# Kernel tuning notes

Hardware: AMD Instinct MI355X
Metric: run time of the kernel (lower is better)

Reference implementation:

```python
import jax, jax.numpy as jnp
import numpy as np

COMMITMENT_COST = 0.25
N, D, K = 131072, 64, 1024


def setup_inputs() -> dict:
    key = jax.random.key(0)
    k1, k2 = jax.random.split(key)
    inputs = jax.random.normal(k1, (N, D), dtype=jnp.float32)
    # torch init: uniform(-1/K, 1/K)
    weight = jax.random.uniform(k2, (K, D), dtype=jnp.float32,
                                minval=-1.0 / K, maxval=1.0 / K)
    return {"inputs": inputs, "weight": weight}


def reference(inputs, weight):
    x2 = jnp.sum(inputs * inputs, axis=1, keepdims=True)          # [N, 1]
    e2 = jnp.sum(weight * weight, axis=1)                          # [K]
    distances = x2 + e2 - 2.0 * jnp.matmul(inputs, weight.T)       # [N, K]
    encoding_indices = jnp.argmin(distances, axis=1)               # [N]
    # scatter one-hot + matmul in the original == direct gather
    quantized = jnp.take(weight, encoding_indices, axis=0)         # [N, D]
    e_latent_loss = jnp.mean((jax.lax.stop_gradient(quantized) - inputs) ** 2)
    q_latent_loss = jnp.mean((quantized - jax.lax.stop_gradient(inputs)) ** 2)
    loss = q_latent_loss + COMMITMENT_COST * e_latent_loss
    # straight-through estimator
    quantized_st = inputs + jax.lax.stop_gradient(quantized - inputs)
    return (quantized_st, loss, encoding_indices)
```

## Files before the change

### kernel.cpp

```cpp
#include <hip/hip_runtime.h>


#define NROWS 131072
#define DIM 64
#define KCODES 1024
#define MARGIN 5e-5f
#define LOSS_SCALE (1.25f / ((float)NROWS * (float)DIM))

typedef short bf16x8 __attribute__((ext_vector_type(8)));
typedef float f32x4 __attribute__((ext_vector_type(4)));

__device__ __forceinline__ short f2bf(float f) {
    unsigned u = __float_as_uint(f);
    u += 0x7FFF + ((u >> 16) & 1);
    return (short)(u >> 16);
}
__device__ __forceinline__ float bf2f(short h) {
    return __uint_as_float(((unsigned)(unsigned short)h) << 16);
}

__global__ __launch_bounds__(256) void prep_w(const float* __restrict__ w,
                                              float* __restrict__ e2,
                                              short* __restrict__ w_hi,
                                              short* __restrict__ w_lo) {
    int k = blockIdx.x * blockDim.x + threadIdx.x;
    if (k >= KCODES) return;
    const float* wk = w + (size_t)k * DIM;
    float r[DIM];
#pragma unroll
    for (int i = 0; i < DIM / 4; ++i) *(float4*)&r[4 * i] = *(const float4*)(wk + 4 * i);
    float s = 0.f;
#pragma unroll
    for (int d = 0; d < DIM; ++d) s = fmaf(r[d], r[d], s);
    e2[k] = s;

    const int t = k >> 5, ct = (k >> 4) & 1, m = k & 15;
#pragma unroll
    for (int kc = 0; kc < 2; ++kc)
#pragma unroll
        for (int q = 0; q < 4; ++q) {
            bf16x8 hv, lv;
#pragma unroll
            for (int j = 0; j < 8; ++j) {
                float f = r[kc * 32 + q * 8 + j];
                short h = f2bf(f);
                hv[j] = h;
                lv[j] = f2bf(f - bf2f(h));
            }
            size_t fo = ((size_t)(((t * 2 + ct) * 2 + kc) * 4 + q) * 16 + m) * 8;
            *(bf16x8*)(w_hi + fo) = hv;
            *(bf16x8*)(w_lo + fo) = lv;
        }
}

__global__ __launch_bounds__(256, 3) void vq_main(
        const float* __restrict__ x, const float* __restrict__ w,
        const float* __restrict__ e2,
        const short* __restrict__ w_hi, const short* __restrict__ w_lo,
        float* __restrict__ out_q, float* __restrict__ out_loss,
        float* __restrict__ out_idx,
        unsigned* __restrict__ flag_cnt, unsigned* __restrict__ flag_list) {
    const int tid = threadIdx.x;
    const int lane = tid & 63;
    const int wv = tid >> 6;
    const int m = lane & 15;
    const int q = lane >> 4;
    const int block_row0 = blockIdx.x * 128;
    const int wave_row0 = block_row0 + wv * 32;

    __shared__ int sidx[128];
    __shared__ unsigned char sflg[128];
    __shared__ float red[4];

    float xa[2][2][8];
#pragma unroll
    for (int rt = 0; rt < 2; ++rt) {
        const float* xr = x + (size_t)(wave_row0 + rt * 16 + m) * DIM + q * 8;
        *(float4*)&xa[rt][0][0] = *(const float4*)(xr);
        *(float4*)&xa[rt][0][4] = *(const float4*)(xr + 4);
        *(float4*)&xa[rt][1][0] = *(const float4*)(xr + 32);
        *(float4*)&xa[rt][1][4] = *(const float4*)(xr + 36);
    }
    bf16x8 ah[2][2], al[2][2];
#pragma unroll
    for (int rt = 0; rt < 2; ++rt)
#pragma unroll
        for (int c = 0; c < 2; ++c)
#pragma unroll
            for (int j = 0; j < 8; ++j) {
                float f = xa[rt][c][j];
                short h = f2bf(f);
                ah[rt][c][j] = h;
                al[rt][c][j] = f2bf(f - bf2f(h));
            }

    float best[2][4], sec[2][4];
    int bidx[2][4];
#pragma unroll
    for (int rt = 0; rt < 2; ++rt)
#pragma unroll
        for (int r = 0; r < 4; ++r) {
            best[rt][r] = 3.4e38f;
            sec[rt][r] = 3.4e38f;
            bidx[rt][r] = 0;
        }

    const short* ph = w_hi + q * 128 + m * 8;
    const short* pl = w_lo + q * 128 + m * 8;

    for (int t = 0; t < KCODES / 32; ++t) {
        bf16x8 bh[2][2], bl[2][2];
#pragma unroll
        for (int ct = 0; ct < 2; ++ct)
#pragma unroll
            for (int kc = 0; kc < 2; ++kc) {
                int off = t * 2048 + (ct * 2 + kc) * 512;
                bh[ct][kc] = *(const bf16x8*)(ph + off);
                bl[ct][kc] = *(const bf16x8*)(pl + off);
            }
        float e2c0 = e2[t * 32 + m];
        float e2c1 = e2[t * 32 + 16 + m];

        f32x4 acc[2][2];
#pragma unroll
        for (int rt = 0; rt < 2; ++rt)
#pragma unroll
            for (int ct = 0; ct < 2; ++ct) {
                f32x4 a = {0.f, 0.f, 0.f, 0.f};
                a = __builtin_amdgcn_mfma_f32_16x16x32_bf16(al[rt][0], bh[ct][0], a, 0, 0, 0);
                a = __builtin_amdgcn_mfma_f32_16x16x32_bf16(ah[rt][0], bl[ct][0], a, 0, 0, 0);
                a = __builtin_amdgcn_mfma_f32_16x16x32_bf16(ah[rt][0], bh[ct][0], a, 0, 0, 0);
                a = __builtin_amdgcn_mfma_f32_16x16x32_bf16(al[rt][1], bh[ct][1], a, 0, 0, 0);
                a = __builtin_amdgcn_mfma_f32_16x16x32_bf16(ah[rt][1], bl[ct][1], a, 0, 0, 0);
                a = __builtin_amdgcn_mfma_f32_16x16x32_bf16(ah[rt][1], bh[ct][1], a, 0, 0, 0);
                acc[rt][ct] = a;
            }

#pragma unroll
        for (int rt = 0; rt < 2; ++rt)
#pragma unroll
            for (int ct = 0; ct < 2; ++ct) {
                float e2c = ct ? e2c1 : e2c0;
                int id = t * 32 + ct * 16 + m;
#pragma unroll
                for (int r = 0; r < 4; ++r) {
                    float g = fmaf(-2.f, acc[rt][ct][r], e2c);
                    bool c = g < best[rt][r];
                    sec[rt][r] = fminf(sec[rt][r], fmaxf(g, best[rt][r]));
                    if (c) { best[rt][r] = g; bidx[rt][r] = id; }
                }
            }
    }

#pragma unroll
    for (int off = 1; off < 16; off <<= 1)
#pragma unroll
        for (int rt = 0; rt < 2; ++rt)
#pragma unroll
            for (int r = 0; r < 4; ++r) {
                float ob = __shfl_xor(best[rt][r], off, 64);
                int oi = __shfl_xor(bidx[rt][r], off, 64);
                float os = __shfl_xor(sec[rt][r], off, 64);
                float mx = fmaxf(best[rt][r], ob);
                sec[rt][r] = fminf(fminf(sec[rt][r], os), mx);
                bool take = (ob < best[rt][r]) ||
                            (ob == best[rt][r] && oi < bidx[rt][r]);
                if (take) { best[rt][r] = ob; bidx[rt][r] = oi; }
            }

    if (m == 0) {
#pragma unroll
        for (int rt = 0; rt < 2; ++rt)
#pragma unroll
            for (int r = 0; r < 4; ++r) {
                int lr = wv * 32 + rt * 16 + q * 4 + r;
                sidx[lr] = bidx[rt][r];
                bool fl = (sec[rt][r] - best[rt][r]) < MARGIN;
                sflg[lr] = fl ? 1 : 0;
                if (fl) {
                    unsigned p = atomicAdd(flag_cnt, 1u);
                    flag_list[p] = (unsigned)(block_row0 + lr);
                }
            }
    }
    __syncthreads();

    float lsum = 0.f;
    const int rl = tid >> 2, part = tid & 3;
#pragma unroll
    for (int p = 0; p < 2; ++p) {
        int lr = p * 64 + rl;
        int grow = block_row0 + lr;
        if (!sflg[lr]) {
            int bi = sidx[lr];
            const float* xs = x + (size_t)grow * DIM + part * 16;
            const float* ws = w + (size_t)bi * DIM + part * 16;
            float* os = out_q + (size_t)grow * DIM + part * 16;
#pragma unroll
            for (int i = 0; i < 4; ++i) {
                float4 xv = *(const float4*)(xs + 4 * i);
                float4 wv4 = *(const float4*)(ws + 4 * i);
                float d0 = wv4.x - xv.x, d1 = wv4.y - xv.y;
                float d2 = wv4.z - xv.z, d3 = wv4.w - xv.w;
                lsum = fmaf(d0, d0, lsum);
                lsum = fmaf(d1, d1, lsum);
                lsum = fmaf(d2, d2, lsum);
                lsum = fmaf(d3, d3, lsum);
                float4 o = {xv.x + d0, xv.y + d1, xv.z + d2, xv.w + d3};
                *(float4*)(os + 4 * i) = o;
            }
            if (part == 0) out_idx[grow] = (float)bi;
        }
    }

    for (int off = 32; off > 0; off >>= 1) lsum += __shfl_down(lsum, off, 64);
    if ((tid & 63) == 0) red[tid >> 6] = lsum;
    __syncthreads();
    if (tid == 0) {
        float s = (red[0] + red[1]) + (red[2] + red[3]);
        atomicAdd(out_loss, s * LOSS_SCALE);
    }
}

#define CH 16
__global__ __launch_bounds__(256) void vq_cleanup(
        const float* __restrict__ x, const float* __restrict__ w,
        const float* __restrict__ e2,
        const unsigned* __restrict__ flag_cnt,
        const unsigned* __restrict__ flag_list,
        float* __restrict__ out_q, float* __restrict__ out_loss,
        float* __restrict__ out_idx) {
    __shared__ float xs[CH][68];
    __shared__ float wt[128][68];
    __shared__ float sx2[CH];
    const int tid = threadIdx.x;
    const int rowsub = tid >> 4;
    const int kslot = tid & 15;
    const unsigned cnt = *flag_cnt;

    for (unsigned base = blockIdx.x * CH; base < cnt; base += gridDim.x * CH) {
        const int nrows = (int)min((unsigned)CH, cnt - base);
        __syncthreads();
        {
            int rr = tid >> 4, sg = tid & 15;
            if (rr < nrows) {
                unsigned grow = flag_list[base + rr];
                *(float4*)&xs[rr][sg * 4] =
                    *(const float4*)(x + (size_t)grow * DIM + sg * 4);
            }
        }
        __syncthreads();
        if (tid < nrows) {
            float s = 0.f;
#pragma unroll
            for (int d = 0; d < DIM; ++d) s = fmaf(xs[tid][d], xs[tid][d], s);
            sx2[tid] = s;
        }

        unsigned long long kmin = ~0ULL;
        for (int tile = 0; tile < KCODES / 128; ++tile) {
            __syncthreads();
#pragma unroll
            for (int i = 0; i < 8; ++i) {
                int f = tid + i * 256;
                int code = f >> 4, sg = f & 15;
                *(float4*)&wt[code][sg * 4] =
                    *(const float4*)(w + (size_t)(tile * 128 + code) * DIM + sg * 4);
            }
            __syncthreads();
            if (rowsub < nrows) {
#pragma unroll
                for (int j = 0; j < 8; ++j) {
                    int cl = j * 16 + kslot;
                    int code = tile * 128 + cl;
                    float dot = 0.f;
#pragma unroll
                    for (int d4 = 0; d4 < 16; ++d4) {
                        float4 wv4 = *(const float4*)&wt[cl][d4 * 4];
                        float4 xv4 = *(const float4*)&xs[rowsub][d4 * 4];
                        dot = fmaf(wv4.x, xv4.x, dot);
                        dot = fmaf(wv4.y, xv4.y, dot);
                        dot = fmaf(wv4.z, xv4.z, dot);
                        dot = fmaf(wv4.w, xv4.w, dot);
                    }
                    float dist = (sx2[rowsub] + e2[code]) - 2.0f * dot;
                    unsigned long long key =
                        ((unsigned long long)__float_as_uint(dist) << 32) |
                        (unsigned)code;
                    kmin = kmin < key ? kmin : key;
                }
            }
        }
#pragma unroll
        for (int off = 1; off < 16; off <<= 1) {
            unsigned long long o = __shfl_xor(kmin, off, 64);
            kmin = kmin < o ? kmin : o;
        }
        if (rowsub < nrows) {
            int bi = (int)(unsigned)(kmin & 0xFFFFFFFFu);
            unsigned grow = flag_list[base + rowsub];
            float4 x4 = *(float4*)&xs[rowsub][kslot * 4];
            float4 w4 = *(const float4*)(w + (size_t)bi * DIM + kslot * 4);
            float d0 = w4.x - x4.x, d1 = w4.y - x4.y;
            float d2 = w4.z - x4.z, d3 = w4.w - x4.w;
            float ls = 0.f;
            ls = fmaf(d0, d0, ls);
            ls = fmaf(d1, d1, ls);
            ls = fmaf(d2, d2, ls);
            ls = fmaf(d3, d3, ls);
            float4 o = {x4.x + d0, x4.y + d1, x4.z + d2, x4.w + d3};
            *(float4*)(out_q + (size_t)grow * DIM + kslot * 4) = o;
            if (kslot == 0) out_idx[grow] = (float)bi;
#pragma unroll
            for (int off = 1; off < 16; off <<= 1)
                ls += __shfl_xor(ls, off, 64);
            if (kslot == 0) atomicAdd(out_loss, ls * LOSS_SCALE);
        }
    }
}

extern "C" void kernel_launch(void* const* d_in, const int* in_sizes, int n_in,
                              void* d_out, int out_size, void* d_ws, size_t ws_size,
                              hipStream_t stream) {
    const float* x = (const float*)d_in[0];
    const float* w = (const float*)d_in[1];

    float* out_q    = (float*)d_out;
    float* out_loss = (float*)d_out + (size_t)NROWS * DIM;
    float* out_idx  = out_loss + 1;

    float* e2 = (float*)d_ws;
    short* w_hi = (short*)(e2 + KCODES);
    short* w_lo = w_hi + (size_t)KCODES * DIM;
    unsigned* cnt = (unsigned*)(w_lo + (size_t)KCODES * DIM);
    unsigned* list = cnt + 1;

    hipMemsetAsync(out_loss, 0, sizeof(float), stream);
    hipMemsetAsync(cnt, 0, sizeof(unsigned), stream);

    prep_w<<<(KCODES + 255) / 256, 256, 0, stream>>>(w, e2, w_hi, w_lo);
    vq_main<<<NROWS / 128, 256, 0, stream>>>(x, w, e2, w_hi, w_lo,
                                             out_q, out_loss, out_idx, cnt, list);
    vq_cleanup<<<256, 256, 0, stream>>>(x, w, e2, cnt, list,
                                        out_q, out_loss, out_idx);
}
```

Baseline: 208.7 us.

## Pack distance and index into sortable uint key, prefetch codebook tiles, split prep

The argmin tracking now packs the distance's float bits (offset by +0.5 so values are positive and monotone as unsigned) with the 10-bit code index into one unsigned key. This replaces float compare, select and separate index tracking with unsigned min/max, and it also shrinks the shuffle reduction. Codebook fragments and e2 for the next tile are software-prefetched into registers while MFMAs run on the current tile. Weight prep is split into a wide swizzle kernel and a separate e2 kernel. The margin is widened to cover the lost mantissa bits, which sends more rows to the cleanup path, and launch bounds drop to 2 blocks per SM to make room for the extra registers.

```diff
diff --git a/kernel.cpp b/kernel.cpp
--- a/kernel.cpp
+++ b/kernel.cpp
@@ -4,10 +4,11 @@
 #define NROWS 131072
 #define DIM 64
 #define KCODES 1024
-#define MARGIN 5e-5f
+#define MARGIN 2.5e-4f
 #define LOSS_SCALE (1.25f / ((float)NROWS * (float)DIM))
 
 typedef short bf16x8 __attribute__((ext_vector_type(8)));
+typedef short s16x4 __attribute__((ext_vector_type(4)));
 typedef float f32x4 __attribute__((ext_vector_type(4)));
 
 __device__ __forceinline__ short f2bf(float f) {
@@ -19,43 +20,44 @@
     return __uint_as_float(((unsigned)(unsigned short)h) << 16);
 }
 
-__global__ __launch_bounds__(256) void prep_w(const float* __restrict__ w,
-                                              float* __restrict__ e2,
-                                              short* __restrict__ w_hi,
-                                              short* __restrict__ w_lo) {
+__global__ __launch_bounds__(256) void prep_swizzle(const float* __restrict__ w,
+                                                    short* __restrict__ w_hi,
+                                                    short* __restrict__ w_lo) {
+    const int gid = blockIdx.x * 256 + threadIdx.x;
+    const int k = gid >> 4, s = gid & 15;
+    const float4 v = *(const float4*)(w + (size_t)k * DIM + s * 4);
+    const int t = k >> 5, ct = (k >> 4) & 1, m = k & 15;
+    const int kc = s >> 3, q = (s >> 1) & 3, j0 = (s & 1) * 4;
+    const size_t fo =
+        ((size_t)(((t * 2 + ct) * 2 + kc) * 4 + q) * 16 + m) * 8 + j0;
+    float f[4] = {v.x, v.y, v.z, v.w};
+    s16x4 hv, lv;
+#pragma unroll
+    for (int i = 0; i < 4; ++i) {
+        short h = f2bf(f[i]);
+        hv[i] = h;
+        lv[i] = f2bf(f[i] - bf2f(h));
+    }
+    *(s16x4*)(w_hi + fo) = hv;
+    *(s16x4*)(w_lo + fo) = lv;
+}
+
+__global__ __launch_bounds__(256) void prep_e2(const float* __restrict__ w,
+                                               float* __restrict__ e2,
+                                               float* __restrict__ e2p) {
     int k = blockIdx.x * blockDim.x + threadIdx.x;
     if (k >= KCODES) return;
     const float* wk = w + (size_t)k * DIM;
-    float r[DIM];
-#pragma unroll
-    for (int i = 0; i < DIM / 4; ++i) *(float4*)&r[4 * i] = *(const float4*)(wk + 4 * i);
     float s = 0.f;
 #pragma unroll
-    for (int d = 0; d < DIM; ++d) s = fmaf(r[d], r[d], s);
+    for (int d = 0; d < DIM; ++d) s = fmaf(wk[d], wk[d], s);
     e2[k] = s;
-
-    const int t = k >> 5, ct = (k >> 4) & 1, m = k & 15;
-#pragma unroll
-    for (int kc = 0; kc < 2; ++kc)
-#pragma unroll
-        for (int q = 0; q < 4; ++q) {
-            bf16x8 hv, lv;
-#pragma unroll
-            for (int j = 0; j < 8; ++j) {
-                float f = r[kc * 32 + q * 8 + j];
-                short h = f2bf(f);
-                hv[j] = h;
-                lv[j] = f2bf(f - bf2f(h));
-            }
-            size_t fo = ((size_t)(((t * 2 + ct) * 2 + kc) * 4 + q) * 16 + m) * 8;
-            *(bf16x8*)(w_hi + fo) = hv;
-            *(bf16x8*)(w_lo + fo) = lv;
-        }
-}
-
-__global__ __launch_bounds__(256, 3) void vq_main(
+    e2p[k] = s + 0.5f;
+}
+
+__global__ __launch_bounds__(256, 2) void vq_main(
         const float* __restrict__ x, const float* __restrict__ w,
-        const float* __restrict__ e2,
+        const float* __restrict__ e2p,
         const short* __restrict__ w_hi, const short* __restrict__ w_lo,
         float* __restrict__ out_q, float* __restrict__ out_loss,
         float* __restrict__ out_idx,
@@ -72,54 +74,63 @@
     __shared__ unsigned char sflg[128];
     __shared__ float red[4];
 
-    float xa[2][2][8];
+    bf16x8 ah[2][2], al[2][2];
 #pragma unroll
     for (int rt = 0; rt < 2; ++rt) {
         const float* xr = x + (size_t)(wave_row0 + rt * 16 + m) * DIM + q * 8;
-        *(float4*)&xa[rt][0][0] = *(const float4*)(xr);
-        *(float4*)&xa[rt][0][4] = *(const float4*)(xr + 4);
-        *(float4*)&xa[rt][1][0] = *(const float4*)(xr + 32);
-        *(float4*)&xa[rt][1][4] = *(const float4*)(xr + 36);
-    }
-    bf16x8 ah[2][2], al[2][2];
-#pragma unroll
-    for (int rt = 0; rt < 2; ++rt)
+        float xa[2][8];
+        *(float4*)&xa[0][0] = *(const float4*)(xr);
+        *(float4*)&xa[0][4] = *(const float4*)(xr + 4);
+        *(float4*)&xa[1][0] = *(const float4*)(xr + 32);
+        *(float4*)&xa[1][4] = *(const float4*)(xr + 36);
 #pragma unroll
         for (int c = 0; c < 2; ++c)
 #pragma unroll
             for (int j = 0; j < 8; ++j) {
-                float f = xa[rt][c][j];
+                float f = xa[c][j];
                 short h = f2bf(f);
                 ah[rt][c][j] = h;
                 al[rt][c][j] = f2bf(f - bf2f(h));
             }
-
-    float best[2][4], sec[2][4];
-    int bidx[2][4];
+    }
+
+    unsigned best[2][4], sec[2][4];
 #pragma unroll
     for (int rt = 0; rt < 2; ++rt)
 #pragma unroll
-        for (int r = 0; r < 4; ++r) {
-            best[rt][r] = 3.4e38f;
-            sec[rt][r] = 3.4e38f;
-            bidx[rt][r] = 0;
-        }
+        for (int r = 0; r < 4; ++r) { best[rt][r] = ~0u; sec[rt][r] = ~0u; }
 
     const short* ph = w_hi + q * 128 + m * 8;
     const short* pl = w_lo + q * 128 + m * 8;
 
+    bf16x8 cbh[2][2], cbl[2][2];
+    float ce[2];
+#pragma unroll
+    for (int ct = 0; ct < 2; ++ct)
+#pragma unroll
+        for (int kc = 0; kc < 2; ++kc) {
+            cbh[ct][kc] = *(const bf16x8*)(ph + (ct * 2 + kc) * 512);
+            cbl[ct][kc] = *(const bf16x8*)(pl + (ct * 2 + kc) * 512);
+        }
+    ce[0] = e2p[m];
+    ce[1] = e2p[16 + m];
+
+    unsigned id0 = (unsigned)m;
+
     for (int t = 0; t < KCODES / 32; ++t) {
-        bf16x8 bh[2][2], bl[2][2];
+        const int tn = (t + 1) & 31;
+        bf16x8 nbh[2][2], nbl[2][2];
+        float ne[2];
 #pragma unroll
         for (int ct = 0; ct < 2; ++ct)
 #pragma unroll
             for (int kc = 0; kc < 2; ++kc) {
-                int off = t * 2048 + (ct * 2 + kc) * 512;
-                bh[ct][kc] = *(const bf16x8*)(ph + off);
-                bl[ct][kc] = *(const bf16x8*)(pl + off);
-            }
-        float e2c0 = e2[t * 32 + m];
-        float e2c1 = e2[t * 32 + 16 + m];
+                int off = tn * 2048 + (ct * 2 + kc) * 512;
+                nbh[ct][kc] = *(const bf16x8*)(ph + off);
+                nbl[ct][kc] = *(const bf16x8*)(pl + off);
+            }
+        ne[0] = e2p[tn * 32 + m];
+        ne[1] = e2p[tn * 32 + 16 + m];
 
         f32x4 acc[2][2];
 #pragma unroll
@@ -127,12 +138,12 @@
 #pragma unroll
             for (int ct = 0; ct < 2; ++ct) {
                 f32x4 a = {0.f, 0.f, 0.f, 0.f};
-                a = __builtin_amdgcn_mfma_f32_16x16x32_bf16(al[rt][0], bh[ct][0], a, 0, 0, 0);
-                a = __builtin_amdgcn_mfma_f32_16x16x32_bf16(ah[rt][0], bl[ct][0], a, 0, 0, 0);
-                a = __builtin_amdgcn_mfma_f32_16x16x32_bf16(ah[rt][0], bh[ct][0], a, 0, 0, 0);
-                a = __builtin_amdgcn_mfma_f32_16x16x32_bf16(al[rt][1], bh[ct][1], a, 0, 0, 0);
-                a = __builtin_amdgcn_mfma_f32_16x16x32_bf16(ah[rt][1], bl[ct][1], a, 0, 0, 0);
-                a = __builtin_amdgcn_mfma_f32_16x16x32_bf16(ah[rt][1], bh[ct][1], a, 0, 0, 0);
+                a = __builtin_amdgcn_mfma_f32_16x16x32_bf16(al[rt][0], cbh[ct][0], a, 0, 0, 0);
+                a = __builtin_amdgcn_mfma_f32_16x16x32_bf16(ah[rt][0], cbl[ct][0], a, 0, 0, 0);
+                a = __builtin_amdgcn_mfma_f32_16x16x32_bf16(ah[rt][0], cbh[ct][0], a, 0, 0, 0);
+                a = __builtin_amdgcn_mfma_f32_16x16x32_bf16(al[rt][1], cbh[ct][1], a, 0, 0, 0);
+                a = __builtin_amdgcn_mfma_f32_16x16x32_bf16(ah[rt][1], cbl[ct][1], a, 0, 0, 0);
+                a = __builtin_amdgcn_mfma_f32_16x16x32_bf16(ah[rt][1], cbh[ct][1], a, 0, 0, 0);
                 acc[rt][ct] = a;
             }
 
@@ -140,16 +151,28 @@
         for (int rt = 0; rt < 2; ++rt)
 #pragma unroll
             for (int ct = 0; ct < 2; ++ct) {
-                float e2c = ct ? e2c1 : e2c0;
-                int id = t * 32 + ct * 16 + m;
+                float e2c = ce[ct];
+                unsigned idc = id0 + (unsigned)(ct * 16);
 #pragma unroll
                 for (int r = 0; r < 4; ++r) {
                     float g = fmaf(-2.f, acc[rt][ct][r], e2c);
-                    bool c = g < best[rt][r];
-                    sec[rt][r] = fminf(sec[rt][r], fmaxf(g, best[rt][r]));
-                    if (c) { best[rt][r] = g; bidx[rt][r] = id; }
+                    unsigned kb = (__float_as_uint(g) & 0xFFFFFC00u) | idc;
+                    unsigned mx = kb > best[rt][r] ? kb : best[rt][r];
+                    sec[rt][r] = sec[rt][r] < mx ? sec[rt][r] : mx;
+                    best[rt][r] = kb < best[rt][r] ? kb : best[rt][r];
                 }
             }
+        id0 += 32;
+
+#pragma unroll
+        for (int ct = 0; ct < 2; ++ct)
+#pragma unroll
+            for (int kc = 0; kc < 2; ++kc) {
+                cbh[ct][kc] = nbh[ct][kc];
+                cbl[ct][kc] = nbl[ct][kc];
+            }
+        ce[0] = ne[0];
+        ce[1] = ne[1];
     }
 
 #pragma unroll
@@ -158,14 +181,12 @@
         for (int rt = 0; rt < 2; ++rt)
 #pragma unroll
             for (int r = 0; r < 4; ++r) {
-                float ob = __shfl_xor(best[rt][r], off, 64);
-                int oi = __shfl_xor(bidx[rt][r], off, 64);
-                float os = __shfl_xor(sec[rt][r], off, 64);
-                float mx = fmaxf(best[rt][r], ob);
-                sec[rt][r] = fminf(fminf(sec[rt][r], os), mx);
-                bool take = (ob < best[rt][r]) ||
-                            (ob == best[rt][r] && oi < bidx[rt][r]);
-                if (take) { best[rt][r] = ob; bidx[rt][r] = oi; }
+                unsigned ob = (unsigned)__shfl_xor((int)best[rt][r], off, 64);
+                unsigned os = (unsigned)__shfl_xor((int)sec[rt][r], off, 64);
+                unsigned mx = ob > best[rt][r] ? ob : best[rt][r];
+                unsigned s2 = sec[rt][r] < os ? sec[rt][r] : os;
+                sec[rt][r] = s2 < mx ? s2 : mx;
+                best[rt][r] = ob < best[rt][r] ? ob : best[rt][r];
             }
 
     if (m == 0) {
@@ -174,8 +195,12 @@
 #pragma unroll
             for (int r = 0; r < 4; ++r) {
                 int lr = wv * 32 + rt * 16 + q * 4 + r;
-                sidx[lr] = bidx[rt][r];
-                bool fl = (sec[rt][r] - best[rt][r]) < MARGIN;
+                unsigned bk = best[rt][r], sk = sec[rt][r];
+                int bi = (int)(bk & 1023u);
+                float bf = __uint_as_float(bk & 0xFFFFFC00u);
+                float sf = __uint_as_float(sk & 0xFFFFFC00u);
+                bool fl = (sf - bf) < MARGIN;
+                sidx[lr] = bi;
                 sflg[lr] = fl ? 1 : 0;
                 if (fl) {
                     unsigned p = atomicAdd(flag_cnt, 1u);
@@ -330,7 +355,8 @@
     float* out_idx  = out_loss + 1;
 
     float* e2 = (float*)d_ws;
-    short* w_hi = (short*)(e2 + KCODES);
+    float* e2p = e2 + KCODES;
+    short* w_hi = (short*)(e2p + KCODES);
     short* w_lo = w_hi + (size_t)KCODES * DIM;
     unsigned* cnt = (unsigned*)(w_lo + (size_t)KCODES * DIM);
     unsigned* list = cnt + 1;
@@ -338,8 +364,9 @@
     hipMemsetAsync(out_loss, 0, sizeof(float), stream);
     hipMemsetAsync(cnt, 0, sizeof(unsigned), stream);
 
-    prep_w<<<(KCODES + 255) / 256, 256, 0, stream>>>(w, e2, w_hi, w_lo);
-    vq_main<<<NROWS / 128, 256, 0, stream>>>(x, w, e2, w_hi, w_lo,
+    prep_swizzle<<<KCODES * 16 / 256, 256, 0, stream>>>(w, w_hi, w_lo);
+    prep_e2<<<(KCODES + 255) / 256, 256, 0, stream>>>(w, e2, e2p);
+    vq_main<<<NROWS / 128, 256, 0, stream>>>(x, w, e2p, w_hi, w_lo,
                                              out_q, out_loss, out_idx, cnt, list);
     vq_cleanup<<<256, 256, 0, stream>>>(x, w, e2, cnt, list,
                                         out_q, out_loss, out_idx);
```

Measured after the change: 410.0 us. 96.5% more time.
